# Optimization experiments

Measured on AMD Instinct MI355X. Metric: run time of the kernel, lower is better.

Reference implementation:

```python
import jax, jax.numpy as jnp
import numpy as np

B, S, HID = 2, 2048, 2048
H, HKV, D = 16, 4, 128

def _rope(x, cos, sin):
    # x: [B,h,S,D]; cos/sin: [1,1,S,D//2]
    d = x.shape[-1] // 2
    x1, x2 = x[..., :d], x[..., d:]
    y1 = x1 * cos + x2 * sin
    y2 = -x1 * sin + x2 * cos
    return jnp.concatenate([y1, y2], axis=-1)

def _rmsnorm(x):
    eps = jnp.finfo(x.dtype).eps
    return x * jax.lax.rsqrt(jnp.mean(jnp.square(x), axis=-1, keepdims=True) + eps)

def setup_inputs() -> dict:
    key = jax.random.key(0)
    ks = jax.random.split(key, 5)
    x = jax.random.normal(ks[0], (B, S, HID), dtype=jnp.float32)
    # realistic rotary tables
    half = D // 2
    inv_freq = 1.0 / (10000.0 ** (jnp.arange(half, dtype=jnp.float32) / half))
    t = jnp.arange(S, dtype=jnp.float32)
    freqs = t[:, None] * inv_freq[None, :]            # [S, D//2]
    cos = jnp.cos(freqs)[None, None]                  # [1,1,S,D//2]
    sin = jnp.sin(freqs)[None, None]
    s = 0.02
    Wq = jax.random.normal(ks[1], (H * D, HID), dtype=jnp.float32) * s
    Wk = jax.random.normal(ks[2], (HKV * D, HID), dtype=jnp.float32) * s
    Wv = jax.random.normal(ks[3], (HKV * D, HID), dtype=jnp.float32) * s
    Wo = jax.random.normal(ks[4], (HID, H * D), dtype=jnp.float32) * s
    return {"x": x, "cos": cos, "sin": sin, "Wq": Wq, "Wk": Wk, "Wv": Wv, "Wo": Wo}

def reference(x, cos, sin, Wq, Wk, Wv, Wo):
    b, s, _ = x.shape
    rep = H // HKV
    q = (x @ Wq.T).reshape(b, s, H, D).transpose(0, 2, 1, 3)      # [B,H,S,D]
    k = (x @ Wk.T).reshape(b, s, HKV, D).transpose(0, 2, 1, 3)    # [B,Hkv,S,D]
    v = (x @ Wv.T).reshape(b, s, HKV, D).transpose(0, 2, 1, 3)
    k = jnp.repeat(k, rep, axis=1)                                # GQA expand
    v = jnp.repeat(v, rep, axis=1)
    q = _rmsnorm(_rope(q, cos, sin))
    k = _rmsnorm(_rope(k, cos, sin))
    scores = jnp.einsum('bhqd,bhkd->bhqk', q, k) * (D ** -0.5)
    causal = jnp.tril(jnp.ones((s, s), dtype=bool))
    scores = jnp.where(causal, scores, -jnp.inf)
    attn = jax.nn.softmax(scores, axis=-1)
    out = jnp.einsum('bhqk,bhkd->bhqd', attn, v)                  # [B,H,S,D]
    out = out.transpose(0, 2, 1, 3).reshape(b, s, H * D)
    return out @ Wo.T
```

## Files before the change

### kernel.cpp

```cpp
#include <hip/hip_runtime.h>
#include <hip/hip_bf16.h>

#define B_  2
#define S_  2048
#define HID_ 2048
#define H_  16
#define HKV_ 4
#define D_  128

typedef __bf16 bf16_t;
typedef bf16_t bf16x8 __attribute__((ext_vector_type(8)));
typedef float f32x4 __attribute__((ext_vector_type(4)));

typedef __attribute__((address_space(3))) unsigned int lds_u32_t;
typedef const __attribute__((address_space(1))) unsigned int glob_u32_t;

__device__ __forceinline__ void gl2lds16(const bf16_t* g, bf16_t* l) {
    __builtin_amdgcn_global_load_lds((glob_u32_t*)g, (lds_u32_t*)l, 16, 0, 0);
}

__device__ __forceinline__ unsigned packbf2(float a, float b) {
    union { bf16_t h[2]; unsigned u; } p;
    p.h[0] = (bf16_t)a;
    p.h[1] = (bf16_t)b;
    return p.u;
}

__global__ void detect_dtype(const unsigned* __restrict__ x, int* __restrict__ flag) {
    int lane = threadIdx.x;
    int c = 0;
#pragma unroll
    for (int i = 0; i < 16; ++i) {
        unsigned w = x[lane * 16 + i];
        unsigned e = (w >> 7) & 0xFF;
        c += (e >= 117 && e <= 137) ? 1 : 0;
    }
#pragma unroll
    for (int m = 1; m < 64; m <<= 1) c += __shfl_xor(c, m, 64);
    if (lane == 0) *flag = (c >= 512) ? 1 : 0;
}

struct Cseg { const void* src; bf16_t* dst; int n8; };

__global__ __launch_bounds__(256) void convert_bf16(Cseg s0, Cseg s1, Cseg s2, Cseg s3,
                                                    const int* __restrict__ flagp) {
    Cseg s = (blockIdx.y == 0) ? s0 : (blockIdx.y == 1) ? s1 : (blockIdx.y == 2) ? s2 : s3;
    const int i = blockIdx.x * 256 + threadIdx.x;
    if (i >= s.n8) return;
    if (*flagp) {
        ((uint4*)s.dst)[i] = ((const uint4*)s.src)[i];
    } else {
        const float4* p = (const float4*)s.src + (size_t)i * 2;
        float4 u = p[0], v = p[1];
        bf16x8 r;
        r[0] = (bf16_t)u.x; r[1] = (bf16_t)u.y; r[2] = (bf16_t)u.z; r[3] = (bf16_t)u.w;
        r[4] = (bf16_t)v.x; r[5] = (bf16_t)v.y; r[6] = (bf16_t)v.z; r[7] = (bf16_t)v.w;
        *(bf16x8*)(s.dst + (size_t)i * 8) = r;
    }
}

__global__ __launch_bounds__(256) void gemm_lds(const bf16_t* __restrict__ A,
                                                const bf16_t* __restrict__ W,
                                                void* __restrict__ C,
                                                int M, int N, int K,
                                                const int* __restrict__ flagp, int osel) {
    __shared__ bf16_t As[128 * 32];
    __shared__ bf16_t Bs[128 * 32];

    const int tid = threadIdx.x;
    const int w = tid >> 6;
    const int lane = tid & 63;
    const int r = lane & 15;
    const int quad = lane >> 4;
    const int m0 = blockIdx.y * 128;
    const int n0 = blockIdx.x * 128;
    const bool of32 = osel && (*flagp == 0);

    const int mh = (w & 1) * 64;
    const int nh = (w >> 1) * 64;

    const int c0 = w * 2;
    const int srow = lane >> 2;
    const int scol = (lane & 3) * 8;
    const bf16_t* Ag0 = A + (size_t)(m0 + c0 * 16 + srow) * K + scol;
    const bf16_t* Ag1 = A + (size_t)(m0 + c0 * 16 + 16 + srow) * K + scol;
    const bf16_t* Wg0 = W + (size_t)(n0 + c0 * 16 + srow) * K + scol;
    const bf16_t* Wg1 = W + (size_t)(n0 + c0 * 16 + 16 + srow) * K + scol;
    bf16_t* Al0 = As + c0 * 512;
    bf16_t* Al1 = As + (c0 + 1) * 512;
    bf16_t* Bl0 = Bs + c0 * 512;
    bf16_t* Bl1 = Bs + (c0 + 1) * 512;

    f32x4 acc[4][4] = {};

    for (int k0 = 0; k0 < K; k0 += 32) {
        __syncthreads();
        gl2lds16(Ag0 + k0, Al0);
        gl2lds16(Ag1 + k0, Al1);
        gl2lds16(Wg0 + k0, Bl0);
        gl2lds16(Wg1 + k0, Bl1);
        __syncthreads();

        bf16x8 a[4], b[4];
#pragma unroll
        for (int mi = 0; mi < 4; ++mi)
            a[mi] = *(const bf16x8*)&As[(mh + mi * 16 + r) * 32 + quad * 8];
#pragma unroll
        for (int ni = 0; ni < 4; ++ni)
            b[ni] = *(const bf16x8*)&Bs[(nh + ni * 16 + r) * 32 + quad * 8];
#pragma unroll
        for (int mi = 0; mi < 4; ++mi)
#pragma unroll
            for (int ni = 0; ni < 4; ++ni)
                acc[mi][ni] = __builtin_amdgcn_mfma_f32_16x16x32_bf16(a[mi], b[ni], acc[mi][ni], 0, 0, 0);
    }

#pragma unroll
    for (int mi = 0; mi < 4; ++mi) {
#pragma unroll
        for (int ni = 0; ni < 4; ++ni) {
#pragma unroll
            for (int g = 0; g < 4; ++g) {
                const int row = m0 + mh + mi * 16 + quad * 4 + g;
                const int col = n0 + nh + ni * 16 + r;
                if (of32) ((float*)C)[(size_t)row * N + col] = acc[mi][ni][g];
                else ((__hip_bfloat16*)C)[(size_t)row * N + col] = __float2bfloat16(acc[mi][ni][g]);
            }
        }
    }
}

template <bool F32>
__device__ __forceinline__ bf16x8 load8(const void* base, size_t off) {
    bf16x8 r;
    if constexpr (F32) {
        const float4* p = (const float4*)((const float*)base + off);
        float4 u = p[0], v = p[1];
        r[0] = (bf16_t)u.x; r[1] = (bf16_t)u.y; r[2] = (bf16_t)u.z; r[3] = (bf16_t)u.w;
        r[4] = (bf16_t)v.x; r[5] = (bf16_t)v.y; r[6] = (bf16_t)v.z; r[7] = (bf16_t)v.w;
    } else {
        r = *(const bf16x8*)((const bf16_t*)base + off);
    }
    return r;
}

template <bool AF32, bool WF32, bool OF32>
__device__ __forceinline__ void gemm_body(const void* __restrict__ A, const void* __restrict__ W,
                                          void* __restrict__ C, int M, int N, int K) {
    const int wave = threadIdx.x >> 6;
    const int lane = threadIdx.x & 63;
    const int r = lane & 15;
    const int quad = lane >> 4;
    const int m0 = blockIdx.y * 64 + wave * 16;
    const int n0 = blockIdx.x * 64;

    f32x4 acc[4] = {};
    const size_t aoff = (size_t)(m0 + r) * K + quad * 8;
    const size_t woff = (size_t)(n0 + r) * K + quad * 8;

    for (int k0 = 0; k0 < K; k0 += 32) {
        bf16x8 a = load8<AF32>(A, aoff + k0);
#pragma unroll
        for (int ns = 0; ns < 4; ++ns) {
            bf16x8 b = load8<WF32>(W, woff + (size_t)(ns * 16) * K + k0);
            acc[ns] = __builtin_amdgcn_mfma_f32_16x16x32_bf16(a, b, acc[ns], 0, 0, 0);
        }
    }

#pragma unroll
    for (int ns = 0; ns < 4; ++ns) {
#pragma unroll
        for (int reg = 0; reg < 4; ++reg) {
            int m = m0 + quad * 4 + reg;
            int n = n0 + ns * 16 + r;
            if constexpr (OF32) ((float*)C)[(size_t)m * N + n] = acc[ns][reg];
            else ((__hip_bfloat16*)C)[(size_t)m * N + n] = __float2bfloat16(acc[ns][reg]);
        }
    }
}

__global__ __launch_bounds__(256) void gemm_bt(const void* __restrict__ A, const void* __restrict__ W,
                                               void* __restrict__ C, int M, int N, int K,
                                               const int* __restrict__ flagp, int mode) {
    const int bf = *flagp;
    if (bf) {
        gemm_body<false, false, false>(A, W, C, M, N, K);
    } else if (mode == 0) {
        gemm_body<true, true, false>(A, W, C, M, N, K);
    } else {
        gemm_body<false, true, true>(A, W, C, M, N, K);
    }
}

__global__ __launch_bounds__(256) void rope_rms(__hip_bfloat16* __restrict__ qk,
                                                const void* __restrict__ cosp,
                                                const void* __restrict__ sinp,
                                                int NH, int ld, const int* __restrict__ flagp) {
    const int bf = *flagp;
    const int wave = threadIdx.x >> 6;
    const int lane = threadIdx.x & 63;
    const int row = blockIdx.x * 4 + wave;
    const int h = row % NH;
    const int bs = row / NH;
    const int s = bs % S_;

    __hip_bfloat16* p = qk + (size_t)bs * ld + h * D_;
    float x1 = __bfloat162float(p[lane]);
    float x2 = __bfloat162float(p[lane + 64]);
    float c, sn, eps;
    if (bf) {
        c   = __bfloat162float(((const __hip_bfloat16*)cosp)[s * 64 + lane]);
        sn  = __bfloat162float(((const __hip_bfloat16*)sinp)[s * 64 + lane]);
        eps = 0.0078125f;
    } else {
        c   = ((const float*)cosp)[s * 64 + lane];
        sn  = ((const float*)sinp)[s * 64 + lane];
        eps = 1.1920929e-07f;
    }
    float y1 = x1 * c + x2 * sn;
    float y2 = x2 * c - x1 * sn;
    float ss = y1 * y1 + y2 * y2;
#pragma unroll
    for (int m = 1; m < 64; m <<= 1) ss += __shfl_xor(ss, m, 64);
    float rinv = rsqrtf(ss * (1.0f / 128.0f) + eps);
    p[lane]      = __float2bfloat16(y1 * rinv);
    p[lane + 64] = __float2bfloat16(y2 * rinv);
}

__global__ __launch_bounds__(256) void k_pack(const __hip_bfloat16* __restrict__ Kin,
                                              bf16_t* __restrict__ Kp) {
    const int idx = blockIdx.x * 256 + threadIdx.x;
    const int d0 = (idx & 15) * 8;
    const int row = (idx >> 4) & 31;
    const int kt = (idx >> 9) & 63;
    const int gy = idx >> 15;
    const int kvh = gy & 3;
    const int bb = gy >> 2;
    const bf16_t* src = (const bf16_t*)Kin + (size_t)(bb * S_ + kt * 32 + row) * 3072 + kvh * D_ + d0;
    *(uint4*)(Kp + (size_t)idx * 8) = *(const uint4*)src;
}

__global__ __launch_bounds__(256) void v_pack(const __hip_bfloat16* __restrict__ V,
                                              unsigned* __restrict__ Vp, int ldv) {
    const int idx = blockIdx.x * 256 + threadIdx.x;
    const int kp = idx & 15;
    const int d  = (idx >> 4) & 127;
    const int kt = (idx >> 11) & 63;
    const int gy = idx >> 17;
    const int kvh = gy & 3;
    const int b = gy >> 2;
    const unsigned short* p = (const unsigned short*)V
        + (size_t)(b * S_ + 32 * kt + kp) * ldv + kvh * D_ + d;
    unsigned lo = p[0];
    unsigned hi = p[(size_t)16 * ldv];
    Vp[idx] = lo | (hi << 16);
}

#define M0F 16.5f
#define OFP 132

__global__ __launch_bounds__(1024, 4) void attn_flash5(const __hip_bfloat16* __restrict__ Q,
                                                       const bf16_t* __restrict__ Kp,
                                                       const unsigned* __restrict__ Vp,
                                                       __hip_bfloat16* __restrict__ O) {
    __shared__ unsigned Pb[16][2][16][16];
    __shared__ float Of[4][32][OFP];
    __shared__ float Lf[4][2][16];

    const int tid = threadIdx.x;
    const int w = tid >> 6;
    const int lane = tid & 63;
    const int r = lane & 15;
    const int quad = lane >> 4;

    const int id = blockIdx.x;
    const int gy = id & 7;
    const int px = id >> 3;
    const int kvh = gy & 3;
    const int b = gy >> 2;
    const int hh = w & 3;
    const int qd = w >> 2;
    const int h = kvh * 4 + hh;

    const bf16_t* Kg = Kp + (size_t)gy * (64 * 32 * 128);
    const unsigned* Vg = Vp + (size_t)gy * (64 * 128 * 16);

    bf16x8 ones;
#pragma unroll
    for (int j = 0; j < 8; ++j) ones[j] = (bf16_t)1.0f;

    const float SC2 = 0.08838834764831845f * 1.4426950408889634f;

    for (int rep = 0; rep < 2; ++rep) {
        const int qt = rep ? (63 - px) : px;
        const int q0 = qt * 32;
        const int nkt = qt + 1;
        const int ktb = (nkt * qd) >> 2;
        const int kte = (nkt * (qd + 1)) >> 2;

        bf16x8 qf[2][4];
#pragma unroll
        for (int t = 0; t < 2; ++t) {
            const bf16_t* qp = (const bf16_t*)Q + (size_t)(b * S_ + q0 + t * 16 + r) * 3072 + h * D_ + quad * 8;
#pragma unroll
            for (int c = 0; c < 4; ++c) qf[t][c] = *(const bf16x8*)(qp + c * 32);
        }

        f32x4 oacc[2][8] = {};
        f32x4 lacc[2] = {};

        for (int kt = ktb; kt < kte; ++kt) {
            const bf16_t* kp0 = Kg + ((size_t)kt * 32 + r) * 128 + quad * 8;

            f32x4 s0[2] = {}, s1[2] = {};
            __builtin_amdgcn_s_setprio(1);
#pragma unroll
            for (int c = 0; c < 4; ++c) {
                bf16x8 kb0 = *(const bf16x8*)(kp0 + c * 32);
                bf16x8 kb1 = *(const bf16x8*)(kp0 + 16 * 128 + c * 32);
#pragma unroll
                for (int t = 0; t < 2; ++t) {
                    s0[t] = __builtin_amdgcn_mfma_f32_16x16x32_bf16(qf[t][c], kb0, s0[t], 0, 0, 0);
                    s1[t] = __builtin_amdgcn_mfma_f32_16x16x32_bf16(qf[t][c], kb1, s1[t], 0, 0, 0);
                }
            }
            __builtin_amdgcn_s_setprio(0);

            if (kt == qt) {
#pragma unroll
                for (int t = 0; t < 2; ++t)
#pragma unroll
                    for (int g = 0; g < 4; ++g) {
                        const int qrow = q0 + t * 16 + quad * 4 + g;
                        if (kt * 32 + r > qrow)      s0[t][g] = -1e38f;
                        if (kt * 32 + 16 + r > qrow) s1[t][g] = -1e38f;
                    }
            }

#pragma unroll
            for (int t = 0; t < 2; ++t)
#pragma unroll
                for (int g = 0; g < 4; ++g) {
                    const float p0 = exp2f(fmaf(s0[t][g], SC2, -M0F));
                    const float p1 = exp2f(fmaf(s1[t][g], SC2, -M0F));
                    Pb[w][t][quad * 4 + g][(((r >> 2) ^ quad) & 3) * 4 + (r & 3)] = packbf2(p0, p1);
                }

            const int pgrp = ((quad ^ (r >> 2)) & 3) * 4;
            bf16x8 pf0 = *(const bf16x8*)&Pb[w][0][r][pgrp];
            bf16x8 pf1 = *(const bf16x8*)&Pb[w][1][r][pgrp];

            lacc[0] = __builtin_amdgcn_mfma_f32_16x16x32_bf16(pf0, ones, lacc[0], 0, 0, 0);
            lacc[1] = __builtin_amdgcn_mfma_f32_16x16x32_bf16(pf1, ones, lacc[1], 0, 0, 0);

            const unsigned* vp = Vg + ((size_t)kt * 128 + r) * 16 + quad * 4;
            __builtin_amdgcn_s_setprio(1);
#pragma unroll
            for (int ns = 0; ns < 8; ++ns) {
                bf16x8 vf = *(const bf16x8*)(vp + ns * 256);
                oacc[0][ns] = __builtin_amdgcn_mfma_f32_16x16x32_bf16(pf0, vf, oacc[0][ns], 0, 0, 0);
                oacc[1][ns] = __builtin_amdgcn_mfma_f32_16x16x32_bf16(pf1, vf, oacc[1][ns], 0, 0, 0);
            }
            __builtin_amdgcn_s_setprio(0);
        }

        __syncthreads();
        if (qd == 1) {
#pragma unroll
            for (int t = 0; t < 2; ++t) {
                if (r == 0) {
#pragma unroll
                    for (int g = 0; g < 4; ++g) Lf[hh][t][quad * 4 + g] = lacc[t][g];
                }
#pragma unroll
                for (int ns = 0; ns < 8; ++ns)
#pragma unroll
                    for (int g = 0; g < 4; ++g)
                        Of[hh][t * 16 + quad * 4 + g][ns * 16 + r] = oacc[t][ns][g];
            }
        }
        __syncthreads();
        if (qd == 2) {
#pragma unroll
            for (int t = 0; t < 2; ++t) {
                if (r == 0) {
#pragma unroll
                    for (int g = 0; g < 4; ++g) Lf[hh][t][quad * 4 + g] += lacc[t][g];
                }
#pragma unroll
                for (int ns = 0; ns < 8; ++ns)
#pragma unroll
                    for (int g = 0; g < 4; ++g)
                        Of[hh][t * 16 + quad * 4 + g][ns * 16 + r] += oacc[t][ns][g];
            }
        }
        __syncthreads();
        if (qd == 3) {
#pragma unroll
            for (int t = 0; t < 2; ++t) {
                if (r == 0) {
#pragma unroll
                    for (int g = 0; g < 4; ++g) Lf[hh][t][quad * 4 + g] += lacc[t][g];
                }
#pragma unroll
                for (int ns = 0; ns < 8; ++ns)
#pragma unroll
                    for (int g = 0; g < 4; ++g)
                        Of[hh][t * 16 + quad * 4 + g][ns * 16 + r] += oacc[t][ns][g];
            }
        }
        __syncthreads();
        if (qd == 0) {
#pragma unroll
            for (int t = 0; t < 2; ++t) {
#pragma unroll
                for (int g = 0; g < 4; ++g) {
                    const int r16 = quad * 4 + g;
                    const float l = lacc[t][g] + Lf[hh][t][r16];
                    const float inv = 1.0f / l;
                    const int qrow = q0 + t * 16 + r16;
                    __hip_bfloat16* op = O + (size_t)(b * S_ + qrow) * 2048 + h * D_;
#pragma unroll
                    for (int ns = 0; ns < 8; ++ns)
                        op[ns * 16 + r] = __float2bfloat16((oacc[t][ns][g] + Of[hh][t * 16 + r16][ns * 16 + r]) * inv);
                }
            }
        }
    }
}

#define KT_ 32
#define LDK 136

__global__ __launch_bounds__(256, 2) void attn_flash3(const __hip_bfloat16* __restrict__ Q,
                                                      const __hip_bfloat16* __restrict__ K,
                                                      const __hip_bfloat16* __restrict__ V,
                                                      __hip_bfloat16* __restrict__ O,
                                                      int ldq, int ldkv, int ldo) {
    __shared__ unsigned short Ks[KT_][LDK];
    __shared__ unsigned int Vt[D_ * 16];
    __shared__ unsigned int Pb[4][2][16][16];

    const int tid = threadIdx.x;
    const int w = tid >> 6;
    const int lane = tid & 63;
    const int r = lane & 15;
    const int quad = lane >> 4;

    const int gy = blockIdx.y;
    const int kvh = gy % HKV_;
    const int b = gy / HKV_;
    const int qt = b ? blockIdx.x : (gridDim.x - 1 - blockIdx.x);
    const int q0 = qt * 32;
    const int h = kvh * 4 + w;

    bf16x8 qf[2][4];
#pragma unroll
    for (int t = 0; t < 2; ++t) {
        const bf16_t* qp = (const bf16_t*)Q + (size_t)(b * S_ + q0 + t * 16 + r) * ldq + h * D_ + quad * 8;
#pragma unroll
        for (int c = 0; c < 4; ++c) qf[t][c] = *(const bf16x8*)(qp + c * 32);
    }

    f32x4 oacc[2][8] = {};
    f32x4 lacc[2] = {};
    float m_i[2][4];
#pragma unroll
    for (int t = 0; t < 2; ++t)
#pragma unroll
        for (int g = 0; g < 4; ++g) m_i[t][g] = -3e38f;

    const bf16_t* Kg = (const bf16_t*)K + (size_t)b * S_ * ldkv + kvh * D_;
    const bf16_t* Vg = (const bf16_t*)V + (size_t)b * S_ * ldkv + kvh * D_;

    bf16x8 ones;
#pragma unroll
    for (int j = 0; j < 8; ++j) ones[j] = (bf16_t)1.0f;

    const float SC2 = 0.08838834764831845f * 1.4426950408889634f;

    const int skey = tid >> 4;
    const int sdc = tid & 15;
    union U4 { uint4 u; unsigned short s[8]; };
    U4 rk0, rk1, rv0, rv1;
    {
        const size_t o0 = (size_t)skey * ldkv + sdc * 8;
        const size_t o1 = o0 + (size_t)16 * ldkv;
        rk0.u = *(const uint4*)(Kg + o0);
        rk1.u = *(const uint4*)(Kg + o1);
        rv0.u = *(const uint4*)(Vg + o0);
        rv1.u = *(const uint4*)(Vg + o1);
    }

    for (int kt = 0; kt <= qt; ++kt) {
        const int k0 = kt * KT_;
        __syncthreads();
        *(uint4*)&Ks[skey][sdc * 8] = rk0.u;
        *(uint4*)&Ks[skey + 16][sdc * 8] = rk1.u;
#pragma unroll
        for (int j = 0; j < 8; ++j) {
            const int d = sdc * 8 + j;
            const int f = ((j >> 1) & 3) ^ (sdc & 3);
            const int grp = (skey >> 2) ^ f;
            Vt[d * 16 + grp * 4 + (skey & 3)] = (unsigned)rv0.s[j] | ((unsigned)rv1.s[j] << 16);
        }
        __syncthreads();
        if (kt < qt) {
            const size_t o0 = (size_t)(k0 + KT_ + skey) * ldkv + sdc * 8;
            const size_t o1 = o0 + (size_t)16 * ldkv;
            rk0.u = *(const uint4*)(Kg + o0);
            rk1.u = *(const uint4*)(Kg + o1);
            rv0.u = *(const uint4*)(Vg + o0);
            rv1.u = *(const uint4*)(Vg + o1);
        }

        f32x4 s0[2] = {}, s1[2] = {};
#pragma unroll
        for (int c = 0; c < 4; ++c) {
            bf16x8 kb0 = *(const bf16x8*)&Ks[r][c * 32 + quad * 8];
            bf16x8 kb1 = *(const bf16x8*)&Ks[16 + r][c * 32 + quad * 8];
#pragma unroll
            for (int t = 0; t < 2; ++t) {
                s0[t] = __builtin_amdgcn_mfma_f32_16x16x32_bf16(qf[t][c], kb0, s0[t], 0, 0, 0);
                s1[t] = __builtin_amdgcn_mfma_f32_16x16x32_bf16(qf[t][c], kb1, s1[t], 0, 0, 0);
            }
        }

        const bool bnd = (kt == qt);
#pragma unroll
        for (int t = 0; t < 2; ++t) {
            float mt[4];
#pragma unroll
            for (int g = 0; g < 4; ++g) {
                s0[t][g] *= SC2;
                s1[t][g] *= SC2;
                if (bnd) {
                    const int qrow = q0 + t * 16 + quad * 4 + g;
                    if (k0 + r > qrow)      s0[t][g] = -1e38f;
                    if (k0 + 16 + r > qrow) s1[t][g] = -1e38f;
                }
                mt[g] = fmaxf(s0[t][g], s1[t][g]);
            }
#pragma unroll
            for (int msk = 1; msk < 16; msk <<= 1) {
#pragma unroll
                for (int g = 0; g < 4; ++g) mt[g] = fmaxf(mt[g], __shfl_xor(mt[g], msk, 64));
            }
            bool upd = false;
#pragma unroll
            for (int g = 0; g < 4; ++g) upd |= (mt[g] > m_i[t][g]);
            if (__ballot(upd)) {
#pragma unroll
                for (int g = 0; g < 4; ++g) {
                    const float mn = fmaxf(m_i[t][g], mt[g]);
                    const float al = exp2f(m_i[t][g] - mn);
                    m_i[t][g] = mn;
                    lacc[t][g] *= al;
#pragma unroll
                    for (int ns = 0; ns < 8; ++ns) oacc[t][ns][g] *= al;
                }
            }
#pragma unroll
            for (int g = 0; g < 4; ++g) {
                const float p0 = exp2f(s0[t][g] - m_i[t][g]);
                const float p1 = exp2f(s1[t][g] - m_i[t][g]);
                const int row = quad * 4 + g;
                Pb[w][t][row][(((r >> 2) ^ quad) & 3) * 4 + (r & 3)] = packbf2(p0, p1);
            }
        }

        const int pgrp = ((quad ^ (r >> 2)) & 3) * 4;
        bf16x8 pf0 = *(const bf16x8*)&Pb[w][0][r][pgrp];
        bf16x8 pf1 = *(const bf16x8*)&Pb[w][1][r][pgrp];

        lacc[0] = __builtin_amdgcn_mfma_f32_16x16x32_bf16(pf0, ones, lacc[0], 0, 0, 0);
        lacc[1] = __builtin_amdgcn_mfma_f32_16x16x32_bf16(pf1, ones, lacc[1], 0, 0, 0);

#pragma unroll
        for (int ns = 0; ns < 8; ++ns) {
            const int d = ns * 16 + r;
            const int f = ((r >> 1) & 3) ^ ((2 * ns + (r >> 3)) & 3);
            bf16x8 vf = *(const bf16x8*)&Vt[d * 16 + ((quad ^ f) & 3) * 4];
            oacc[0][ns] = __builtin_amdgcn_mfma_f32_16x16x32_bf16(pf0, vf, oacc[0][ns], 0, 0, 0);
            oacc[1][ns] = __builtin_amdgcn_mfma_f32_16x16x32_bf16(pf1, vf, oacc[1][ns], 0, 0, 0);
        }
    }

#pragma unroll
    for (int t = 0; t < 2; ++t) {
#pragma unroll
        for (int g = 0; g < 4; ++g) {
            const float inv = 1.0f / lacc[t][g];
            const int qrow = q0 + t * 16 + quad * 4 + g;
            __hip_bfloat16* op = O + (size_t)(b * S_ + qrow) * ldo + h * D_;
#pragma unroll
            for (int ns = 0; ns < 8; ++ns)
                op[ns * 16 + r] = __float2bfloat16(oacc[t][ns][g] * inv);
        }
    }
}

extern "C" void kernel_launch(void* const* d_in, const int* in_sizes, int n_in,
                              void* d_out, int out_size, void* d_ws, size_t ws_size,
                              hipStream_t stream) {
    const void* x    = d_in[0];
    const void* cosp = d_in[1];
    const void* sinp = d_in[2];
    const void* Wq   = d_in[3];
    const void* Wk   = d_in[4];
    const void* Wv   = d_in[5];
    const void* Wo   = d_in[6];

    const int M = B_ * S_;
    const size_t MB = 1ull << 20;

    if (ws_size >= 28 * MB + 64) {
        char* ws = (char*)d_ws;
        bf16_t* xb = (bf16_t*)ws;
        bf16_t* wb = (bf16_t*)(ws + 16 * MB);
        bf16_t* wo = (bf16_t*)(ws + 16 * MB);
        unsigned* vp4 = (unsigned*)(ws + 24 * MB);
        bf16_t* ao = (bf16_t*)ws;
        int* flag  = (int*)(ws + 28 * MB);
        bf16_t* qkv = (bf16_t*)d_out;
        bf16_t* kp8 = (bf16_t*)((char*)d_out + 24 * MB);

        detect_dtype<<<1, 64, 0, stream>>>((const unsigned*)x, flag);

        Cseg sx{x,  xb,                          (B_ * S_ * HID_) / 8};
        Cseg sq{Wq, wb,                          (H_ * D_ * HID_) / 8};
        Cseg sk{Wk, wb + (size_t)2048 * HID_,    (HKV_ * D_ * HID_) / 8};
        Cseg sv{Wv, wb + (size_t)2560 * HID_,    (HKV_ * D_ * HID_) / 8};
        convert_bf16<<<dim3(4096, 4), 256, 0, stream>>>(sx, sq, sk, sv, flag);

        gemm_lds<<<dim3(3072 / 128, M / 128), 256, 0, stream>>>(xb, wb, qkv, M, 3072, HID_, flag, 0);

        Cseg so{Wo, wo, (HID_ * H_ * D_) / 8};
        convert_bf16<<<dim3(2048, 1), 256, 0, stream>>>(so, so, so, so, flag);

        v_pack<<<(B_ * HKV_ * D_ * 64 * 16) / 256, 256, 0, stream>>>(
            (const __hip_bfloat16*)(qkv + 2560), vp4, 3072);

        rope_rms<<<(B_ * S_ * H_) / 4, 256, 0, stream>>>((__hip_bfloat16*)qkv, cosp, sinp, H_, 3072, flag);
        rope_rms<<<(B_ * S_ * HKV_) / 4, 256, 0, stream>>>((__hip_bfloat16*)(qkv + 2048), cosp, sinp, HKV_, 3072, flag);

        k_pack<<<dim3(1024), 256, 0, stream>>>((const __hip_bfloat16*)(qkv + 2048), kp8);

        attn_flash5<<<dim3(256), 1024, 0, stream>>>(
            (const __hip_bfloat16*)qkv, kp8, vp4, (__hip_bfloat16*)ao);

        gemm_lds<<<dim3(HID_ / 128, M / 128), 256, 0, stream>>>(ao, wo, d_out, M, HID_, H_ * D_, flag, 1);
    } else {
        __hip_bfloat16* qb = (__hip_bfloat16*)d_ws;
        int* flag = (int*)((char*)d_ws + (size_t)M * (H_ * D_) * sizeof(__hip_bfloat16));
        __hip_bfloat16* kb = (__hip_bfloat16*)d_out;
        __hip_bfloat16* vb = kb + (size_t)M * (HKV_ * D_);

        detect_dtype<<<1, 64, 0, stream>>>((const unsigned*)x, flag);

        gemm_bt<<<dim3((H_ * D_) / 64, M / 64), 256, 0, stream>>>(x, Wq, qb, M, H_ * D_, HID_, flag, 0);
        gemm_bt<<<dim3((HKV_ * D_) / 64, M / 64), 256, 0, stream>>>(x, Wk, kb, M, HKV_ * D_, HID_, flag, 0);
        gemm_bt<<<dim3((HKV_ * D_) / 64, M / 64), 256, 0, stream>>>(x, Wv, vb, M, HKV_ * D_, HID_, flag, 0);

        rope_rms<<<(B_ * S_ * H_) / 4, 256, 0, stream>>>(qb, cosp, sinp, H_, H_ * D_, flag);
        rope_rms<<<(B_ * S_ * HKV_) / 4, 256, 0, stream>>>(kb, cosp, sinp, HKV_, HKV_ * D_, flag);

        attn_flash3<<<dim3(S_ / 32, B_ * HKV_), 256, 0, stream>>>(qb, kb, vb, qb, H_ * D_, HKV_ * D_, H_ * D_);

        gemm_bt<<<dim3(HID_ / 64, M / 64), 256, 0, stream>>>(qb, Wo, d_out, M, HID_, H_ * D_, flag, 1);
    }
}
```

Measured before the change: 435.7 us.

## Restructure flash attention to per-wave query tiles with async LDS prefetch

Replaces the 1024-thread attention kernel, which split each query tile's key range across four waves and reduced the partial results through shared memory, with a 512-thread kernel. In the new kernel each wave owns a whole query tile, and tiles are paired to balance causal work. K and V tiles are prefetched into per-wave LDS buffers with global_load_lds and double-issued ahead of compute. The pack kernels now write XOR-swizzled layouts to avoid LDS bank conflicts. This removes the cross-wave reduction and its barriers, at the cost of lower occupancy and more LDS use per block.

```diff
diff --git a/kernel.cpp b/kernel.cpp
--- a/kernel.cpp
+++ b/kernel.cpp
@@ -230,23 +230,27 @@
 __global__ __launch_bounds__(256) void k_pack(const __hip_bfloat16* __restrict__ Kin,
                                               bf16_t* __restrict__ Kp) {
     const int idx = blockIdx.x * 256 + threadIdx.x;
-    const int d0 = (idx & 15) * 8;
+    const int sl = idx & 15;
     const int row = (idx >> 4) & 31;
     const int kt = (idx >> 9) & 63;
     const int gy = idx >> 15;
+    const int slot = sl ^ (row & 15);
     const int kvh = gy & 3;
     const int bb = gy >> 2;
-    const bf16_t* src = (const bf16_t*)Kin + (size_t)(bb * S_ + kt * 32 + row) * 3072 + kvh * D_ + d0;
+    const bf16_t* src = (const bf16_t*)Kin + (size_t)(bb * S_ + kt * 32 + row) * 3072 + kvh * D_ + slot * 8;
     *(uint4*)(Kp + (size_t)idx * 8) = *(const uint4*)src;
 }
 
 __global__ __launch_bounds__(256) void v_pack(const __hip_bfloat16* __restrict__ V,
                                               unsigned* __restrict__ Vp, int ldv) {
     const int idx = blockIdx.x * 256 + threadIdx.x;
-    const int kp = idx & 15;
+    const int j  = idx & 3;
+    const int sl = (idx >> 2) & 3;
     const int d  = (idx >> 4) & 127;
     const int kt = (idx >> 11) & 63;
     const int gy = idx >> 17;
+    const int s  = sl ^ ((d >> 1) & 3);
+    const int kp = s * 4 + j;
     const int kvh = gy & 3;
     const int b = gy >> 2;
     const unsigned short* p = (const unsigned short*)V
@@ -257,15 +261,14 @@
 }
 
 #define M0F 16.5f
-#define OFP 132
-
-__global__ __launch_bounds__(1024, 4) void attn_flash5(const __hip_bfloat16* __restrict__ Q,
-                                                       const bf16_t* __restrict__ Kp,
-                                                       const unsigned* __restrict__ Vp,
-                                                       __hip_bfloat16* __restrict__ O) {
-    __shared__ unsigned Pb[16][2][16][16];
-    __shared__ float Of[4][32][OFP];
-    __shared__ float Lf[4][2][16];
+
+__global__ __launch_bounds__(512, 1) void attn_flash9(const __hip_bfloat16* __restrict__ Q,
+                                                      const bf16_t* __restrict__ Kp,
+                                                      const unsigned* __restrict__ Vp,
+                                                      __hip_bfloat16* __restrict__ O) {
+    __shared__ bf16_t   Kl[8][4096];
+    __shared__ unsigned Vl[8][2048];
+    __shared__ unsigned PbS[8][2][16][16];
 
     const int tid = threadIdx.x;
     const int w = tid >> 6;
@@ -275,15 +278,33 @@
 
     const int id = blockIdx.x;
     const int gy = id & 7;
-    const int px = id >> 3;
+    const int u = id >> 3;
+    const int hh = u & 3;
+    const int i = u >> 2;
     const int kvh = gy & 3;
     const int b = gy >> 2;
-    const int hh = w & 3;
-    const int qd = w >> 2;
     const int h = kvh * 4 + hh;
 
-    const bf16_t* Kg = Kp + (size_t)gy * (64 * 32 * 128);
-    const unsigned* Vg = Vp + (size_t)gy * (64 * 128 * 16);
+    const int s4 = w & 3;
+    int tlo = (s4 == 0) ? i : (s4 == 1) ? (31 - i) : (s4 == 2) ? (16 + i) : (15 - i);
+    const int qt = (w < 4) ? tlo : (63 - tlo);
+    const int q0 = qt * 32;
+
+    const bf16_t* Ksrc = Kp + (size_t)gy * (64 * 4096);
+    const unsigned* Vsrc = Vp + (size_t)gy * (64 * 2048);
+    bf16_t* klds = &Kl[w][0];
+    unsigned* vlds = &Vl[w][0];
+
+    bf16x8 qf[2][4];
+#pragma unroll
+    for (int t = 0; t < 2; ++t) {
+        const bf16_t* qp = (const bf16_t*)Q + (size_t)(b * S_ + q0 + t * 16 + r) * 3072 + h * D_ + quad * 8;
+#pragma unroll
+        for (int c = 0; c < 4; ++c) qf[t][c] = *(const bf16x8*)(qp + c * 32);
+    }
+
+    f32x4 oacc[2][8] = {};
+    f32x4 lacc[2] = {};
 
     bf16x8 ones;
 #pragma unroll
@@ -291,140 +312,98 @@
 
     const float SC2 = 0.08838834764831845f * 1.4426950408889634f;
 
-    for (int rep = 0; rep < 2; ++rep) {
-        const int qt = rep ? (63 - px) : px;
-        const int q0 = qt * 32;
-        const int nkt = qt + 1;
-        const int ktb = (nkt * qd) >> 2;
-        const int kte = (nkt * (qd + 1)) >> 2;
-
-        bf16x8 qf[2][4];
-#pragma unroll
-        for (int t = 0; t < 2; ++t) {
-            const bf16_t* qp = (const bf16_t*)Q + (size_t)(b * S_ + q0 + t * 16 + r) * 3072 + h * D_ + quad * 8;
-#pragma unroll
-            for (int c = 0; c < 4; ++c) qf[t][c] = *(const bf16x8*)(qp + c * 32);
-        }
-
-        f32x4 oacc[2][8] = {};
-        f32x4 lacc[2] = {};
-
-        for (int kt = ktb; kt < kte; ++kt) {
-            const bf16_t* kp0 = Kg + ((size_t)kt * 32 + r) * 128 + quad * 8;
-
-            f32x4 s0[2] = {}, s1[2] = {};
-            __builtin_amdgcn_s_setprio(1);
-#pragma unroll
-            for (int c = 0; c < 4; ++c) {
-                bf16x8 kb0 = *(const bf16x8*)(kp0 + c * 32);
-                bf16x8 kb1 = *(const bf16x8*)(kp0 + 16 * 128 + c * 32);
-#pragma unroll
-                for (int t = 0; t < 2; ++t) {
-                    s0[t] = __builtin_amdgcn_mfma_f32_16x16x32_bf16(qf[t][c], kb0, s0[t], 0, 0, 0);
-                    s1[t] = __builtin_amdgcn_mfma_f32_16x16x32_bf16(qf[t][c], kb1, s1[t], 0, 0, 0);
+    unsigned* pbw = &PbS[w][0][0][0];
+    const int pwi = (((r >> 2) ^ quad) & 3) * 4 + (r & 3);
+    const int pgrp = ((quad ^ (r >> 2)) & 3) * 4;
+    const int vsw = (quad ^ ((r >> 1) & 3)) * 4;
+
+#define ISSUE(KT) do {                                                        \
+        const bf16_t* ks_ = Ksrc + (size_t)(KT) * 4096 + lane * 8;            \
+        const bf16_t* vs_ = (const bf16_t*)(Vsrc + (size_t)(KT) * 2048) + lane * 8; \
+        _Pragma("unroll")                                                     \
+        for (int jj = 0; jj < 8; ++jj) {                                      \
+            gl2lds16(ks_ + jj * 512, klds + jj * 512);                        \
+            gl2lds16(vs_ + jj * 512, (bf16_t*)vlds + jj * 512);               \
+        }                                                                     \
+    } while (0)
+
+    ISSUE(0);
+    for (int kt = 0; kt <= qt; ++kt) {
+        asm volatile("s_waitcnt vmcnt(0)" ::: "memory");
+
+        bf16x8 kf[8], vf[8];
+#pragma unroll
+        for (int c = 0; c < 4; ++c) {
+            const int sA = ((quad + 4 * c) ^ r) * 8;
+            kf[2 * c]     = *(const bf16x8*)&klds[r * 128 + sA];
+            kf[2 * c + 1] = *(const bf16x8*)&klds[(16 + r) * 128 + sA];
+        }
+#pragma unroll
+        for (int ns = 0; ns < 8; ++ns)
+            vf[ns] = *(const bf16x8*)&vlds[(ns * 16 + r) * 16 + vsw];
+
+        asm volatile("s_waitcnt lgkmcnt(0)" ::: "memory");
+        __builtin_amdgcn_sched_barrier(0);
+        if (kt < qt) ISSUE(kt + 1);
+
+        f32x4 s0_[2] = {}, s1_[2] = {};
+        __builtin_amdgcn_s_setprio(1);
+#pragma unroll
+        for (int c = 0; c < 4; ++c) {
+#pragma unroll
+            for (int t = 0; t < 2; ++t) {
+                s0_[t] = __builtin_amdgcn_mfma_f32_16x16x32_bf16(qf[t][c], kf[2 * c], s0_[t], 0, 0, 0);
+                s1_[t] = __builtin_amdgcn_mfma_f32_16x16x32_bf16(qf[t][c], kf[2 * c + 1], s1_[t], 0, 0, 0);
+            }
+        }
+        __builtin_amdgcn_s_setprio(0);
+
+        if (kt == qt) {
+#pragma unroll
+            for (int t = 0; t < 2; ++t)
+#pragma unroll
+                for (int g = 0; g < 4; ++g) {
+                    const int qrow = q0 + t * 16 + quad * 4 + g;
+                    if (kt * 32 + r > qrow)      s0_[t][g] = -1e38f;
+                    if (kt * 32 + 16 + r > qrow) s1_[t][g] = -1e38f;
                 }
-            }
-            __builtin_amdgcn_s_setprio(0);
-
-            if (kt == qt) {
-#pragma unroll
-                for (int t = 0; t < 2; ++t)
-#pragma unroll
-                    for (int g = 0; g < 4; ++g) {
-                        const int qrow = q0 + t * 16 + quad * 4 + g;
-                        if (kt * 32 + r > qrow)      s0[t][g] = -1e38f;
-                        if (kt * 32 + 16 + r > qrow) s1[t][g] = -1e38f;
-                    }
-            }
-
-#pragma unroll
-            for (int t = 0; t < 2; ++t)
-#pragma unroll
-                for (int g = 0; g < 4; ++g) {
-                    const float p0 = exp2f(fmaf(s0[t][g], SC2, -M0F));
-                    const float p1 = exp2f(fmaf(s1[t][g], SC2, -M0F));
-                    Pb[w][t][quad * 4 + g][(((r >> 2) ^ quad) & 3) * 4 + (r & 3)] = packbf2(p0, p1);
-                }
-
-            const int pgrp = ((quad ^ (r >> 2)) & 3) * 4;
-            bf16x8 pf0 = *(const bf16x8*)&Pb[w][0][r][pgrp];
-            bf16x8 pf1 = *(const bf16x8*)&Pb[w][1][r][pgrp];
-
-            lacc[0] = __builtin_amdgcn_mfma_f32_16x16x32_bf16(pf0, ones, lacc[0], 0, 0, 0);
-            lacc[1] = __builtin_amdgcn_mfma_f32_16x16x32_bf16(pf1, ones, lacc[1], 0, 0, 0);
-
-            const unsigned* vp = Vg + ((size_t)kt * 128 + r) * 16 + quad * 4;
-            __builtin_amdgcn_s_setprio(1);
-#pragma unroll
-            for (int ns = 0; ns < 8; ++ns) {
-                bf16x8 vf = *(const bf16x8*)(vp + ns * 256);
-                oacc[0][ns] = __builtin_amdgcn_mfma_f32_16x16x32_bf16(pf0, vf, oacc[0][ns], 0, 0, 0);
-                oacc[1][ns] = __builtin_amdgcn_mfma_f32_16x16x32_bf16(pf1, vf, oacc[1][ns], 0, 0, 0);
-            }
-            __builtin_amdgcn_s_setprio(0);
-        }
-
-        __syncthreads();
-        if (qd == 1) {
-#pragma unroll
-            for (int t = 0; t < 2; ++t) {
-                if (r == 0) {
-#pragma unroll
-                    for (int g = 0; g < 4; ++g) Lf[hh][t][quad * 4 + g] = lacc[t][g];
-                }
-#pragma unroll
-                for (int ns = 0; ns < 8; ++ns)
-#pragma unroll
-                    for (int g = 0; g < 4; ++g)
-                        Of[hh][t * 16 + quad * 4 + g][ns * 16 + r] = oacc[t][ns][g];
-            }
-        }
-        __syncthreads();
-        if (qd == 2) {
-#pragma unroll
-            for (int t = 0; t < 2; ++t) {
-                if (r == 0) {
-#pragma unroll
-                    for (int g = 0; g < 4; ++g) Lf[hh][t][quad * 4 + g] += lacc[t][g];
-                }
-#pragma unroll
-                for (int ns = 0; ns < 8; ++ns)
-#pragma unroll
-                    for (int g = 0; g < 4; ++g)
-                        Of[hh][t * 16 + quad * 4 + g][ns * 16 + r] += oacc[t][ns][g];
-            }
-        }
-        __syncthreads();
-        if (qd == 3) {
-#pragma unroll
-            for (int t = 0; t < 2; ++t) {
-                if (r == 0) {
-#pragma unroll
-                    for (int g = 0; g < 4; ++g) Lf[hh][t][quad * 4 + g] += lacc[t][g];
-                }
-#pragma unroll
-                for (int ns = 0; ns < 8; ++ns)
-#pragma unroll
-                    for (int g = 0; g < 4; ++g)
-                        Of[hh][t * 16 + quad * 4 + g][ns * 16 + r] += oacc[t][ns][g];
-            }
-        }
-        __syncthreads();
-        if (qd == 0) {
-#pragma unroll
-            for (int t = 0; t < 2; ++t) {
-#pragma unroll
-                for (int g = 0; g < 4; ++g) {
-                    const int r16 = quad * 4 + g;
-                    const float l = lacc[t][g] + Lf[hh][t][r16];
-                    const float inv = 1.0f / l;
-                    const int qrow = q0 + t * 16 + r16;
-                    __hip_bfloat16* op = O + (size_t)(b * S_ + qrow) * 2048 + h * D_;
-#pragma unroll
-                    for (int ns = 0; ns < 8; ++ns)
-                        op[ns * 16 + r] = __float2bfloat16((oacc[t][ns][g] + Of[hh][t * 16 + r16][ns * 16 + r]) * inv);
-                }
-            }
+        }
+
+#pragma unroll
+        for (int t = 0; t < 2; ++t)
+#pragma unroll
+            for (int g = 0; g < 4; ++g) {
+                const float p0 = exp2f(fmaf(s0_[t][g], SC2, -M0F));
+                const float p1 = exp2f(fmaf(s1_[t][g], SC2, -M0F));
+                pbw[t * 256 + (quad * 4 + g) * 16 + pwi] = packbf2(p0, p1);
+            }
+
+        bf16x8 pf0 = *(const bf16x8*)&pbw[r * 16 + pgrp];
+        bf16x8 pf1 = *(const bf16x8*)&pbw[256 + r * 16 + pgrp];
+
+        lacc[0] = __builtin_amdgcn_mfma_f32_16x16x32_bf16(pf0, ones, lacc[0], 0, 0, 0);
+        lacc[1] = __builtin_amdgcn_mfma_f32_16x16x32_bf16(pf1, ones, lacc[1], 0, 0, 0);
+
+        __builtin_amdgcn_s_setprio(1);
+#pragma unroll
+        for (int ns = 0; ns < 8; ++ns) {
+            oacc[0][ns] = __builtin_amdgcn_mfma_f32_16x16x32_bf16(pf0, vf[ns], oacc[0][ns], 0, 0, 0);
+            oacc[1][ns] = __builtin_amdgcn_mfma_f32_16x16x32_bf16(pf1, vf[ns], oacc[1][ns], 0, 0, 0);
+        }
+        __builtin_amdgcn_s_setprio(0);
+    }
+#undef ISSUE
+
+#pragma unroll
+    for (int t = 0; t < 2; ++t) {
+#pragma unroll
+        for (int g = 0; g < 4; ++g) {
+            const float inv = 1.0f / lacc[t][g];
+            const int qrow = q0 + t * 16 + quad * 4 + g;
+            __hip_bfloat16* op = O + (size_t)(b * S_ + qrow) * 2048 + h * D_;
+#pragma unroll
+            for (int ns = 0; ns < 8; ++ns)
+                op[ns * 16 + r] = __float2bfloat16(oacc[t][ns][g] * inv);
         }
     }
 }
@@ -646,7 +625,7 @@
 
         k_pack<<<dim3(1024), 256, 0, stream>>>((const __hip_bfloat16*)(qkv + 2048), kp8);
 
-        attn_flash5<<<dim3(256), 1024, 0, stream>>>(
+        attn_flash9<<<dim3(256), 512, 0, stream>>>(
             (const __hip_bfloat16*)qkv, kp8, vp4, (__hip_bfloat16*)ao);
 
         gemm_lds<<<dim3(HID_ / 128, M / 128), 256, 0, stream>>>(ao, wo, d_out, M, HID_, H_ * D_, flag, 1);
```

New measurement: 349.3 us. -19.8%, faster.
